# Optimization experiments

Hardware: AMD Instinct MI355X
Metric: run time of the kernel (lower is better)

The kernel has to match this reference:

```python
import jax, jax.numpy as jnp
import numpy as np

B, T, V, H, E, MAX_OOV = 128, 200, 50257, 256, 128, 50


def setup_inputs() -> dict:
    key = jax.random.key(0)
    ks = jax.random.split(key, 17)
    s = 0.05  # param scale
    return {
        "decoder_input": jax.random.randint(ks[0], (B, 1), 0, V),
        "encoder_outputs": jax.random.normal(ks[1], (B, T, 2 * H), jnp.float32),
        "encoder_idxs": jax.random.randint(ks[2], (B, T), 0, V),
        "prev_state": jax.random.normal(ks[3], (1, B, H), jnp.float32),
        "selective_read": jax.random.normal(ks[4], (B, 1, 2 * H), jnp.float32) * s,
        "step": 1,
        "emb": jax.random.normal(ks[5], (V, E), jnp.float32) * s,
        "W_ih": jax.random.normal(ks[6], (3 * H, E + 2 * H), jnp.float32) * s,
        "W_hh": jax.random.normal(ks[7], (3 * H, H), jnp.float32) * s,
        "b_ih": jax.random.normal(ks[8], (3 * H,), jnp.float32) * s,
        "b_hh": jax.random.normal(ks[9], (3 * H,), jnp.float32) * s,
        "Wi_w": jax.random.normal(ks[10], (H, 2 * H), jnp.float32) * s,
        "Wi_b": jax.random.normal(ks[11], (H,), jnp.float32) * s,
        "Wg_w": jax.random.normal(ks[12], (V, H), jnp.float32) * s,
        "Wg_b": jax.random.normal(ks[13], (V,), jnp.float32) * s,
        "Wc_w": jax.random.normal(ks[14], (H, 2 * H), jnp.float32) * s,
        "Wc_b": jax.random.normal(ks[15], (H,), jnp.float32) * s,
    }


def _gru_cell(x, h, W_ih, W_hh, b_ih, b_hh):
    # torch GRUCell math, gate order r,z,n
    gi = x @ W_ih.T + b_ih
    gh = h @ W_hh.T + b_hh
    i_r, i_z, i_n = jnp.split(gi, 3, axis=-1)
    h_r, h_z, h_n = jnp.split(gh, 3, axis=-1)
    r = jax.nn.sigmoid(i_r + h_r)
    z = jax.nn.sigmoid(i_z + h_z)
    n = jnp.tanh(i_n + r * h_n)
    return (1.0 - z) * n + z * h


def reference(decoder_input, encoder_outputs, encoder_idxs, prev_state, selective_read,
              step, emb, W_ih, W_hh, b_ih, b_hh, Wi_w, Wi_b, Wg_w, Wg_b, Wc_w, Wc_b):
    dtype = encoder_outputs.dtype
    if step == 0:
        prev_state = (encoder_outputs[:, -1] @ Wi_w.T + Wi_b)[None]      # 1,B,H
        selective_read = jnp.zeros((B, 1, 2 * H), dtype)
    embedded = emb[decoder_input[:, 0]]                                   # B,E
    gru_in = jnp.concatenate([selective_read[:, 0], embedded], axis=-1)   # B,2H+E
    decode_hidden = _gru_cell(gru_in, prev_state[0], W_ih, W_hh, b_ih, b_hh)  # B,H

    score_g = decode_hidden @ Wg_w.T + Wg_b                               # B,V
    enc_proj = jnp.tanh(jnp.einsum('bte,he->bth', encoder_outputs, Wc_w) + Wc_b)  # B,T,H
    score_c = jnp.tanh(jnp.einsum('bth,bh->bt', enc_proj, decode_hidden))         # B,T
    score_c = score_c + jnp.where(encoder_idxs == 0, -10000.0, 0.0).astype(dtype)

    probs = jax.nn.softmax(jnp.concatenate([score_g, score_c], axis=1), axis=1)   # B,V+T
    prob_g, prob_c = probs[:, :V], probs[:, V:]
    prob_g = jnp.concatenate([prob_g, jnp.full((B, MAX_OOV), 1e-4, dtype)], axis=1)  # B,V+oov

    # copy-distribution aggregation: scatter-add prob_c by vocab id (replaces one-hot bmm)
    prob_c_to_g = jnp.zeros((B, V + MAX_OOV), dtype).at[
        jnp.arange(B)[:, None], encoder_idxs].add(prob_c)
    prob_out = (prob_c_to_g + prob_g)[:, None, :]                          # B,1,V+oov

    # selective read for next step
    match = (encoder_idxs == decoder_input).astype(dtype)                  # B,T
    tot = match.sum(axis=1, keepdims=True)
    match = jnp.where(tot > 1, match / tot, match)
    prob_appeared = prob_c * match
    selective_read_new = jnp.einsum('bt,bte->be', prob_appeared, encoder_outputs)[:, None, :]  # B,1,2H
    return prob_out, decode_hidden, selective_read_new
```

## Files before the change

kernel.cpp:

```cpp
#include <hip/hip_runtime.h>

typedef __bf16 bf16;
typedef __bf16 bf16x8 __attribute__((ext_vector_type(8)));
typedef float f32x4 __attribute__((ext_vector_type(4)));

#define B_ 128
#define T_ 200
#define V_ 50257
#define H_ 256
#define E_ 128
#define OOV_ 50
#define VO_ 50307
#define NRG 80
#define NTS 5
#define GSC 629
#define TILES_G 3145
#define PSTR 3152
#define GPJ 400

__device__ __forceinline__ float sigmoid_(float x) { return 1.0f / (1.0f + __expf(-x)); }
__device__ __forceinline__ float tanh_(float x) { return 1.0f - 2.0f / (__expf(2.0f * x) + 1.0f); }

__global__ void k_front(const float* Wc_w, bf16* WcPack,
                        const int* step_p, const float* enc, const float* prev,
                        const float* selread, const int* dec, const float* emb,
                        const float* Wi_w, const float* Wi_b,
                        float* hT, float* ginT) {
    if (blockIdx.x < 128) {
        int gid = blockIdx.x * 256 + threadIdx.x;
        int n = gid >> 7;
        int k = (gid & 127) * 4;
        float4 v = *(const float4*)(Wc_w + n * 512 + k);
        int kstep = k >> 5, kin = k & 31;
        int q = kin >> 3, j0 = kin & 7;
        int r = n & 15, nt = n >> 4;
        int lane = q * 16 + r;
        bf16* d = WcPack + (((nt * 16 + kstep) * 64) + lane) * 8 + j0;
        d[0] = (bf16)v.x; d[1] = (bf16)v.y; d[2] = (bf16)v.z; d[3] = (bf16)v.w;
    } else {
        int b = blockIdx.x - 128, t = threadIdx.x;
        int step = step_p[0];
        float h;
        if (step == 0) {
            float acc = Wi_b[t];
            const float* er = enc + (b * T_ + (T_ - 1)) * 512;
            const float* wr = Wi_w + t * 512;
            for (int k = 0; k < 512; ++k) acc += er[k] * wr[k];
            h = acc;
        } else {
            h = prev[b * H_ + t];
        }
        hT[t * B_ + b] = h;
        for (int k = t; k < 512; k += 256)
            ginT[k * B_ + b] = (step == 0) ? 0.0f : selread[b * 512 + k];
        if (t < E_)
            ginT[(512 + t) * B_ + b] = emb[dec[b] * E_ + t];
    }
}

__global__ void k_gemm_gru(const float* W_ih, const float* b_ih,
                           const float* W_hh, const float* b_hh,
                           const float* ginT, const float* hT,
                           float* giT, float* ghT) {
    int g = blockIdx.x * 256 + threadIdx.x;
    int r = g >> 7, b = g & 127;
    const float* w = W_ih + r * 640;
    float a0 = 0.f, a1 = 0.f, a2 = 0.f, a3 = 0.f;
#pragma unroll 4
    for (int k = 0; k < 640; k += 4) {
        a0 += w[k]     * ginT[k * B_ + b];
        a1 += w[k + 1] * ginT[(k + 1) * B_ + b];
        a2 += w[k + 2] * ginT[(k + 2) * B_ + b];
        a3 += w[k + 3] * ginT[(k + 3) * B_ + b];
    }
    giT[r * B_ + b] = b_ih[r] + ((a0 + a1) + (a2 + a3));
    const float* w2 = W_hh + r * 256;
    float c0 = 0.f, c1 = 0.f, c2 = 0.f, c3 = 0.f;
#pragma unroll 4
    for (int k = 0; k < 256; k += 4) {
        c0 += w2[k]     * hT[k * B_ + b];
        c1 += w2[k + 1] * hT[(k + 1) * B_ + b];
        c2 += w2[k + 2] * hT[(k + 2) * B_ + b];
        c3 += w2[k + 3] * hT[(k + 3) * B_ + b];
    }
    ghT[r * B_ + b] = b_hh[r] + ((c0 + c1) + (c2 + c3));
}

__global__ void k_gru_cell(const float* giT, const float* ghT, const float* hT,
                           float* out_dh, bf16* Apack) {
    int b = blockIdx.x, j = threadIdx.x;
    float ir = giT[j * B_ + b], iz = giT[(256 + j) * B_ + b], in_ = giT[(512 + j) * B_ + b];
    float hr = ghT[j * B_ + b], hz = ghT[(256 + j) * B_ + b], hn = ghT[(512 + j) * B_ + b];
    float hp = hT[j * B_ + b];
    float r = sigmoid_(ir + hr);
    float z = sigmoid_(iz + hz);
    float n = tanh_(in_ + r * hn);
    float h = (1.0f - z) * n + z * hp;
    out_dh[b * H_ + j] = h;
    int mt = b >> 4, rr = b & 15, ks = j >> 5, q = (j >> 3) & 3, jj = j & 7;
    Apack[(((mt * 8 + ks) * 64) + (q * 16 + rr)) * 8 + jj] = (bf16)h;
}

__global__ __launch_bounds__(256, 3) void k_mm(const bf16* Apack, const float* Wg_w,
                                               const float* Wg_b, const float* enc,
                                               const bf16* WcPack, const float* Wc_b,
                                               const float* dh, const int* idxs,
                                               float* out_prob, float* pg_part, float* expc) {
    __shared__ unsigned char smem[43008];
    int tid = threadIdx.x;
    int w = tid >> 6, lane = tid & 63;
    int r = lane & 15, q = lane >> 4;
    if (blockIdx.x < GSC) {
        int blk = blockIdx.x;
        int n0 = blk * NRG;
        bf16* Bs = (bf16*)smem;
#pragma unroll
        for (int ph = 0; ph < 2; ++ph) {
            float4 tmp[10];
#pragma unroll
            for (int j = 0; j < 10; ++j) {
                int f = (ph * 10 + j) * 256 + tid;
                int row = f >> 6, c4 = f & 63;
                int n = n0 + row;
                tmp[j] = (n < V_) ? *(const float4*)(Wg_w + n * 256 + c4 * 4)
                                  : float4{0.f, 0.f, 0.f, 0.f};
            }
#pragma unroll
            for (int j = 0; j < 10; ++j) {
                int f = (ph * 10 + j) * 256 + tid;
                int row = f >> 6, c4 = f & 63;
                bf16* d = Bs + row * 264 + c4 * 4;
                d[0] = (bf16)tmp[j].x; d[1] = (bf16)tmp[j].y;
                d[2] = (bf16)tmp[j].z; d[3] = (bf16)tmp[j].w;
            }
        }
        bf16x8 a[2][8];
#pragma unroll
        for (int p = 0; p < 2; ++p)
#pragma unroll
            for (int ks = 0; ks < 8; ++ks)
                a[p][ks] = *(const bf16x8*)(Apack + ((2 * w + p) * 8 + ks) * 512 + lane * 8);
        __syncthreads();
        f32x4 acc[10];
#pragma unroll
        for (int i = 0; i < 10; ++i) acc[i] = (f32x4){0.f, 0.f, 0.f, 0.f};
#pragma unroll
        for (int ks = 0; ks < 8; ++ks) {
#pragma unroll
            for (int nt = 0; nt < NTS; ++nt) {
                bf16x8 bfr = *(const bf16x8*)(Bs + (nt * 16 + r) * 264 + ks * 32 + q * 8);
                acc[nt * 2]     = __builtin_amdgcn_mfma_f32_16x16x32_bf16(a[0][ks], bfr, acc[nt * 2], 0, 0, 0);
                acc[nt * 2 + 1] = __builtin_amdgcn_mfma_f32_16x16x32_bf16(a[1][ks], bfr, acc[nt * 2 + 1], 0, 0, 0);
            }
        }
        __syncthreads();
        float* Tr = (float*)smem;
#pragma unroll
        for (int nt = 0; nt < NTS; ++nt) {
            int n = n0 + nt * 16 + r;
            bool valid = n < V_;
            float wgb = valid ? Wg_b[n] : 0.0f;
#pragma unroll
            for (int p = 0; p < 2; ++p) {
#pragma unroll
                for (int rg = 0; rg < 4; ++rg) {
                    int row = (2 * w + p) * 16 + q * 4 + rg;
                    float e = valid ? __expf(acc[nt * 2 + p][rg] + wgb) : 0.0f;
                    Tr[row * 84 + nt * 16 + r] = e;
                    float sred = e;
                    sred += __shfl_xor(sred, 1);
                    sred += __shfl_xor(sred, 2);
                    sred += __shfl_xor(sred, 4);
                    sred += __shfl_xor(sred, 8);
                    if (r == 0) pg_part[row * PSTR + blk * NTS + nt] = sred;
                }
            }
        }
        __syncthreads();
        if (blk < GSC - 1) {
#pragma unroll
            for (int rnd = 0; rnd < 10; ++rnd) {
                int f = rnd * 256 + tid;
                int row = (f * 3277) >> 16;
                int c4 = f - row * 20;
                float4 v = *(const float4*)(Tr + row * 84 + c4 * 4);
                *(float4*)(out_prob + row * VO_ + n0 + c4 * 4) = v;
            }
        } else {
#pragma unroll
            for (int rnd = 0; rnd < 10; ++rnd) {
                int f = rnd * 256 + tid;
                int row = (f * 3277) >> 16;
                int c4 = f - row * 20;
#pragma unroll
                for (int i = 0; i < 4; ++i) {
                    int n = n0 + c4 * 4 + i;
                    if (n < V_) out_prob[row * VO_ + n] = Tr[row * 84 + c4 * 4 + i];
                }
            }
        }
    } else {
        int pblk = blockIdx.x - GSC;
        int m0 = pblk * 64;
        bf16* As = (bf16*)smem;
        float* sred = (float*)(smem + 33792);
        f32x4 acc[16];
#pragma unroll
        for (int i = 0; i < 16; ++i) acc[i] = (f32x4){0.f, 0.f, 0.f, 0.f};
        for (int half = 0; half < 2; ++half) {
            __syncthreads();
#pragma unroll
            for (int ph = 0; ph < 2; ++ph) {
                float4 tmp[8];
#pragma unroll
                for (int j = 0; j < 8; ++j) {
                    int f = (ph * 8 + j) * 256 + tid;
                    int row = f >> 6, c4 = f & 63;
                    tmp[j] = *(const float4*)(enc + (m0 + row) * 512 + half * 256 + c4 * 4);
                }
#pragma unroll
                for (int j = 0; j < 8; ++j) {
                    int f = (ph * 8 + j) * 256 + tid;
                    int row = f >> 6, c4 = f & 63;
                    bf16* d = As + row * 264 + c4 * 4;
                    d[0] = (bf16)tmp[j].x; d[1] = (bf16)tmp[j].y;
                    d[2] = (bf16)tmp[j].z; d[3] = (bf16)tmp[j].w;
                }
            }
            __syncthreads();
#pragma unroll
            for (int ks = 0; ks < 8; ++ks) {
                int kstep = half * 8 + ks;
                bf16x8 bfr[4];
#pragma unroll
                for (int ntl = 0; ntl < 4; ++ntl)
                    bfr[ntl] = *(const bf16x8*)(WcPack + (((w * 4 + ntl) * 16 + kstep) * 64 + lane) * 8);
#pragma unroll
                for (int mt = 0; mt < 4; ++mt) {
                    bf16x8 a = *(const bf16x8*)(As + (mt * 16 + r) * 264 + ks * 32 + q * 8);
#pragma unroll
                    for (int ntl = 0; ntl < 4; ++ntl)
                        acc[mt * 4 + ntl] = __builtin_amdgcn_mfma_f32_16x16x32_bf16(a, bfr[ntl], acc[mt * 4 + ntl], 0, 0, 0);
                }
            }
        }
#pragma unroll
        for (int mt = 0; mt < 4; ++mt) {
#pragma unroll
            for (int rg = 0; rg < 4; ++rg) {
                int rowl = mt * 16 + q * 4 + rg;
                int row = m0 + rowl;
                int b = row / T_;
                float s = 0.0f;
#pragma unroll
                for (int ntl = 0; ntl < 4; ++ntl) {
                    int n = (w * 4 + ntl) * 16 + r;
                    float pv = tanh_(acc[mt * 4 + ntl][rg] + Wc_b[n]);
                    s += pv * dh[b * H_ + n];
                }
                s += __shfl_xor(s, 1);
                s += __shfl_xor(s, 2);
                s += __shfl_xor(s, 4);
                s += __shfl_xor(s, 8);
                if (r == 0) sred[rowl * 4 + w] = s;
            }
        }
        __syncthreads();
        if (tid < 64) {
            float s = sred[tid * 4] + sred[tid * 4 + 1] + sred[tid * 4 + 2] + sred[tid * 4 + 3];
            int row = m0 + tid;
            int b = row / T_, t = row - b * T_;
            float sc = tanh_(s);
            if (idxs[b * T_ + t] == 0) sc -= 10000.0f;
            expc[row] = __expf(sc);
        }
    }
}

__global__ void k_red_scatter(const float* pg_part, const float* expc_, const int* idxs,
                              const int* dec, const float* enc, float* inv_out,
                              float* out_prob, float* out_sel) {
    __shared__ float red[256];
    __shared__ float cf[256];
    int b = blockIdx.x, t = threadIdx.x;
    float s = 0.0f;
    for (int i = t; i < TILES_G; i += 256) s += pg_part[b * PSTR + i];
    if (t < T_) s += expc_[b * T_ + t];
    red[t] = s;
    __syncthreads();
    for (int k = 128; k > 0; k >>= 1) {
        if (t < k) red[t] += red[t + k];
        __syncthreads();
    }
    float iv = 1.0f / red[0];
    if (t == 0) inv_out[b] = iv;
    __syncthreads();
    int d = dec[b];
    float ec = 0.0f;
    int m = 0;
    if (t < T_) {
        int ix = idxs[b * T_ + t];
        ec = expc_[b * T_ + t];
        atomicAdd(&out_prob[b * VO_ + ix], ec);
        m = (ix == d) ? 1 : 0;
    }
    cf[t] = m ? ec * iv : 0.0f;
    red[t] = m ? 1.0f : 0.0f;
    __syncthreads();
    for (int k = 128; k > 0; k >>= 1) {
        if (t < k) red[t] += red[t + k];
        __syncthreads();
    }
    float tot = red[0];
    float scale = (tot > 1.0f) ? 1.0f / tot : 1.0f;
    float a0 = 0.0f, a1 = 0.0f;
    for (int tt = 0; tt < T_; ++tt) {
        float c = cf[tt];
        if (c != 0.0f) {
            float wgt = c * scale;
            a0 += wgt * enc[(b * T_ + tt) * 512 + t];
            a1 += wgt * enc[(b * T_ + tt) * 512 + t + 256];
        }
    }
    out_sel[b * 512 + t] = a0;
    out_sel[b * 512 + t + 256] = a1;
}

__global__ void k_norm(float* out_prob, const float* inv) {
    int i4 = blockIdx.x * 256 + threadIdx.x;
    if (i4 >= (B_ * VO_ / 4)) return;
    float4 vv = ((const float4*)out_prob)[i4];
    float r[4];
    int base = i4 * 4;
#pragma unroll
    for (int c = 0; c < 4; ++c) {
        int idx = base + c;
        int b = idx / VO_;
        int v = idx - b * VO_;
        float x = (c == 0) ? vv.x : (c == 1) ? vv.y : (c == 2) ? vv.z : vv.w;
        r[c] = (v < V_) ? x * inv[b] : 1e-4f;
    }
    ((float4*)out_prob)[i4] = make_float4(r[0], r[1], r[2], r[3]);
}

extern "C" void kernel_launch(void* const* d_in, const int* in_sizes, int n_in,
                              void* d_out, int out_size, void* d_ws, size_t ws_size,
                              hipStream_t stream) {
    const int*   dec     = (const int*)d_in[0];
    const float* enc     = (const float*)d_in[1];
    const int*   idxs    = (const int*)d_in[2];
    const float* prev    = (const float*)d_in[3];
    const float* selread = (const float*)d_in[4];
    const int*   step_p  = (const int*)d_in[5];
    const float* emb     = (const float*)d_in[6];
    const float* W_ih    = (const float*)d_in[7];
    const float* W_hh    = (const float*)d_in[8];
    const float* b_ih    = (const float*)d_in[9];
    const float* b_hh    = (const float*)d_in[10];
    const float* Wi_w    = (const float*)d_in[11];
    const float* Wi_b    = (const float*)d_in[12];
    const float* Wg_w    = (const float*)d_in[13];
    const float* Wg_b    = (const float*)d_in[14];
    const float* Wc_w    = (const float*)d_in[15];
    const float* Wc_b    = (const float*)d_in[16];

    float* ws     = (float*)d_ws;
    float* hT     = ws;
    float* ginT   = ws + 32768;
    float* giT    = ws + 114688;
    float* ghT    = ws + 212992;
    float* inv    = ws + 311296;
    float* expc   = ws + 311552;
    float* pgp    = ws + 337152;
    bf16*  Apack  = (bf16*)(ws + 741376);
    bf16*  WcPack = (bf16*)(ws + 757760);

    float* out      = (float*)d_out;
    float* out_prob = out;
    float* out_dh   = out + 6439296;
    float* out_sel  = out + 6439296 + 32768;

    k_front<<<256, 256, 0, stream>>>(Wc_w, WcPack, step_p, enc, prev, selread, dec,
                                     emb, Wi_w, Wi_b, hT, ginT);
    k_gemm_gru<<<384, 256, 0, stream>>>(W_ih, b_ih, W_hh, b_hh, ginT, hT, giT, ghT);
    k_gru_cell<<<B_, 256, 0, stream>>>(giT, ghT, hT, out_dh, Apack);
    k_mm<<<GSC + GPJ, 256, 0, stream>>>(Apack, Wg_w, Wg_b, enc, WcPack, Wc_b,
                                        out_dh, idxs, out_prob, pgp, expc);
    k_red_scatter<<<B_, 256, 0, stream>>>(pgp, expc, idxs, dec, enc, inv, out_prob, out_sel);
    k_norm<<<(B_ * VO_ / 4 + 255) / 256, 256, 0, stream>>>(out_prob, inv);
}
```

Before: 271.3 us.

## Make k_mm persistent with double-buffered LDS tiles and register prefetch

Turns the generator-score and copy-projection halves of k_mm into persistent loops over smaller 32-row chunks. Each iteration prefetches the next chunk's fp32 weights or encoder rows into registers while the MFMAs run on the current LDS buffer, then writes them to the other buffer. The launch shrinks to a fixed 1024 blocks and LDS use drops, so the occupancy hint rises from 3 to 4 blocks per CU. The staged LDS transpose before the output store is removed in favour of direct scalar stores of the exponentials, which gives up the coalesced float4 writes.

```diff
diff --git a/kernel.cpp b/kernel.cpp
--- a/kernel.cpp
+++ b/kernel.cpp
@@ -11,12 +11,12 @@
 #define E_ 128
 #define OOV_ 50
 #define VO_ 50307
-#define NRG 80
-#define NTS 5
-#define GSC 629
-#define TILES_G 3145
+#define NCH_S 1571
+#define NCH_P 800
+#define SB 512
+#define PB 512
+#define TILES_G 3142
 #define PSTR 3152
-#define GPJ 400
 
 __device__ __forceinline__ float sigmoid_(float x) { return 1.0f / (1.0f + __expf(-x)); }
 __device__ __forceinline__ float tanh_(float x) { return 1.0f - 2.0f / (__expf(2.0f * x) + 1.0f); }
@@ -101,178 +101,206 @@
     Apack[(((mt * 8 + ks) * 64) + (q * 16 + rr)) * 8 + jj] = (bf16)h;
 }
 
-__global__ __launch_bounds__(256, 3) void k_mm(const bf16* Apack, const float* Wg_w,
+__global__ __launch_bounds__(256, 4) void k_mm(const bf16* Apack, const float* Wg_w,
                                                const float* Wg_b, const float* enc,
                                                const bf16* WcPack, const float* Wc_b,
                                                const float* dh, const int* idxs,
                                                float* out_prob, float* pg_part, float* expc) {
-    __shared__ unsigned char smem[43008];
+    __shared__ unsigned char smem[34816];
+    bf16* buf0 = (bf16*)smem;
+    bf16* buf1 = (bf16*)(smem + 16896);
+    float* sredp = (float*)(smem + 33792);
     int tid = threadIdx.x;
     int w = tid >> 6, lane = tid & 63;
     int r = lane & 15, q = lane >> 4;
-    if (blockIdx.x < GSC) {
+    if (blockIdx.x < SB) {
         int blk = blockIdx.x;
-        int n0 = blk * NRG;
-        bf16* Bs = (bf16*)smem;
-#pragma unroll
-        for (int ph = 0; ph < 2; ++ph) {
-            float4 tmp[10];
-#pragma unroll
-            for (int j = 0; j < 10; ++j) {
-                int f = (ph * 10 + j) * 256 + tid;
+        bf16x8 a[2][8];
+#pragma unroll
+        for (int p = 0; p < 2; ++p)
+#pragma unroll
+            for (int ks = 0; ks < 8; ++ks)
+                a[p][ks] = *(const bf16x8*)(Apack + ((2 * w + p) * 8 + ks) * 512 + lane * 8);
+        {
+            int n0 = blk * 32;
+#pragma unroll
+            for (int j = 0; j < 8; ++j) {
+                int f = j * 256 + tid;
                 int row = f >> 6, c4 = f & 63;
                 int n = n0 + row;
-                tmp[j] = (n < V_) ? *(const float4*)(Wg_w + n * 256 + c4 * 4)
-                                  : float4{0.f, 0.f, 0.f, 0.f};
-            }
-#pragma unroll
-            for (int j = 0; j < 10; ++j) {
-                int f = (ph * 10 + j) * 256 + tid;
-                int row = f >> 6, c4 = f & 63;
-                bf16* d = Bs + row * 264 + c4 * 4;
-                d[0] = (bf16)tmp[j].x; d[1] = (bf16)tmp[j].y;
-                d[2] = (bf16)tmp[j].z; d[3] = (bf16)tmp[j].w;
-            }
-        }
-        bf16x8 a[2][8];
-#pragma unroll
-        for (int p = 0; p < 2; ++p)
-#pragma unroll
-            for (int ks = 0; ks < 8; ++ks)
-                a[p][ks] = *(const bf16x8*)(Apack + ((2 * w + p) * 8 + ks) * 512 + lane * 8);
-        __syncthreads();
-        f32x4 acc[10];
-#pragma unroll
-        for (int i = 0; i < 10; ++i) acc[i] = (f32x4){0.f, 0.f, 0.f, 0.f};
-#pragma unroll
-        for (int ks = 0; ks < 8; ++ks) {
-#pragma unroll
-            for (int nt = 0; nt < NTS; ++nt) {
-                bf16x8 bfr = *(const bf16x8*)(Bs + (nt * 16 + r) * 264 + ks * 32 + q * 8);
-                acc[nt * 2]     = __builtin_amdgcn_mfma_f32_16x16x32_bf16(a[0][ks], bfr, acc[nt * 2], 0, 0, 0);
-                acc[nt * 2 + 1] = __builtin_amdgcn_mfma_f32_16x16x32_bf16(a[1][ks], bfr, acc[nt * 2 + 1], 0, 0, 0);
-            }
-        }
-        __syncthreads();
-        float* Tr = (float*)smem;
-#pragma unroll
-        for (int nt = 0; nt < NTS; ++nt) {
-            int n = n0 + nt * 16 + r;
-            bool valid = n < V_;
-            float wgb = valid ? Wg_b[n] : 0.0f;
-#pragma unroll
-            for (int p = 0; p < 2; ++p) {
-#pragma unroll
-                for (int rg = 0; rg < 4; ++rg) {
-                    int row = (2 * w + p) * 16 + q * 4 + rg;
-                    float e = valid ? __expf(acc[nt * 2 + p][rg] + wgb) : 0.0f;
-                    Tr[row * 84 + nt * 16 + r] = e;
-                    float sred = e;
-                    sred += __shfl_xor(sred, 1);
-                    sred += __shfl_xor(sred, 2);
-                    sred += __shfl_xor(sred, 4);
-                    sred += __shfl_xor(sred, 8);
-                    if (r == 0) pg_part[row * PSTR + blk * NTS + nt] = sred;
-                }
-            }
-        }
-        __syncthreads();
-        if (blk < GSC - 1) {
-#pragma unroll
-            for (int rnd = 0; rnd < 10; ++rnd) {
-                int f = rnd * 256 + tid;
-                int row = (f * 3277) >> 16;
-                int c4 = f - row * 20;
-                float4 v = *(const float4*)(Tr + row * 84 + c4 * 4);
-                *(float4*)(out_prob + row * VO_ + n0 + c4 * 4) = v;
-            }
-        } else {
-#pragma unroll
-            for (int rnd = 0; rnd < 10; ++rnd) {
-                int f = rnd * 256 + tid;
-                int row = (f * 3277) >> 16;
-                int c4 = f - row * 20;
-#pragma unroll
-                for (int i = 0; i < 4; ++i) {
-                    int n = n0 + c4 * 4 + i;
-                    if (n < V_) out_prob[row * VO_ + n] = Tr[row * 84 + c4 * 4 + i];
-                }
-            }
-        }
-    } else {
-        int pblk = blockIdx.x - GSC;
-        int m0 = pblk * 64;
-        bf16* As = (bf16*)smem;
-        float* sred = (float*)(smem + 33792);
-        f32x4 acc[16];
-#pragma unroll
-        for (int i = 0; i < 16; ++i) acc[i] = (f32x4){0.f, 0.f, 0.f, 0.f};
-        for (int half = 0; half < 2; ++half) {
+                float4 v = (n < V_) ? *(const float4*)(Wg_w + n * 256 + c4 * 4)
+                                    : float4{0.f, 0.f, 0.f, 0.f};
+                bf16* d = buf0 + row * 264 + c4 * 4;
+                d[0] = (bf16)v.x; d[1] = (bf16)v.y; d[2] = (bf16)v.z; d[3] = (bf16)v.w;
+            }
+        }
+        int cur = 0;
+        for (int c = blk; c < NCH_S; c += SB) {
+            int n0 = c * 32;
+            int cn = c + SB;
+            bool hn = cn < NCH_S;
+            float4 tmp[8];
+            if (hn) {
+                int n0n = cn * 32;
+#pragma unroll
+                for (int j = 0; j < 8; ++j) {
+                    int f = j * 256 + tid;
+                    int row = f >> 6, c4 = f & 63;
+                    int n = n0n + row;
+                    tmp[j] = (n < V_) ? *(const float4*)(Wg_w + n * 256 + c4 * 4)
+                                      : float4{0.f, 0.f, 0.f, 0.f};
+                }
+            }
             __syncthreads();
-#pragma unroll
-            for (int ph = 0; ph < 2; ++ph) {
-                float4 tmp[8];
+            const bf16* Bq = cur ? buf1 : buf0;
+            f32x4 acc[4];
+#pragma unroll
+            for (int i = 0; i < 4; ++i) acc[i] = (f32x4){0.f, 0.f, 0.f, 0.f};
+#pragma unroll
+            for (int ks = 0; ks < 8; ++ks) {
+#pragma unroll
+                for (int ntl = 0; ntl < 2; ++ntl) {
+                    bf16x8 bfr = *(const bf16x8*)(Bq + (ntl * 16 + r) * 264 + ks * 32 + q * 8);
+                    acc[ntl * 2]     = __builtin_amdgcn_mfma_f32_16x16x32_bf16(a[0][ks], bfr, acc[ntl * 2], 0, 0, 0);
+                    acc[ntl * 2 + 1] = __builtin_amdgcn_mfma_f32_16x16x32_bf16(a[1][ks], bfr, acc[ntl * 2 + 1], 0, 0, 0);
+                }
+            }
+            if (hn) {
+                bf16* Bn = cur ? buf0 : buf1;
 #pragma unroll
                 for (int j = 0; j < 8; ++j) {
-                    int f = (ph * 8 + j) * 256 + tid;
+                    int f = j * 256 + tid;
                     int row = f >> 6, c4 = f & 63;
-                    tmp[j] = *(const float4*)(enc + (m0 + row) * 512 + half * 256 + c4 * 4);
-                }
-#pragma unroll
-                for (int j = 0; j < 8; ++j) {
-                    int f = (ph * 8 + j) * 256 + tid;
-                    int row = f >> 6, c4 = f & 63;
-                    bf16* d = As + row * 264 + c4 * 4;
+                    bf16* d = Bn + row * 264 + c4 * 4;
                     d[0] = (bf16)tmp[j].x; d[1] = (bf16)tmp[j].y;
                     d[2] = (bf16)tmp[j].z; d[3] = (bf16)tmp[j].w;
                 }
             }
+#pragma unroll
+            for (int ntl = 0; ntl < 2; ++ntl) {
+                int n = n0 + ntl * 16 + r;
+                bool valid = n < V_;
+                float wgb = valid ? Wg_b[n] : 0.0f;
+#pragma unroll
+                for (int p = 0; p < 2; ++p) {
+#pragma unroll
+                    for (int rg = 0; rg < 4; ++rg) {
+                        int row = (2 * w + p) * 16 + q * 4 + rg;
+                        float e = valid ? __expf(acc[ntl * 2 + p][rg] + wgb) : 0.0f;
+                        if (valid) out_prob[row * VO_ + n] = e;
+                        float sr = e;
+                        sr += __shfl_xor(sr, 1);
+                        sr += __shfl_xor(sr, 2);
+                        sr += __shfl_xor(sr, 4);
+                        sr += __shfl_xor(sr, 8);
+                        if (r == 0) pg_part[row * PSTR + c * 2 + ntl] = sr;
+                    }
+                }
+            }
+            cur ^= 1;
+        }
+    } else {
+        int pblk = blockIdx.x - SB;
+        int nc = 0;
+        for (int c = pblk; c < NCH_P; c += PB) ++nc;
+        int nhc = nc * 2;
+        {
+            int m0 = pblk * 32;
+#pragma unroll
+            for (int j = 0; j < 8; ++j) {
+                int f = j * 256 + tid;
+                int row = f >> 6, c4 = f & 63;
+                float4 v = *(const float4*)(enc + (m0 + row) * 512 + c4 * 4);
+                bf16* d = buf0 + row * 264 + c4 * 4;
+                d[0] = (bf16)v.x; d[1] = (bf16)v.y; d[2] = (bf16)v.z; d[3] = (bf16)v.w;
+            }
+        }
+        int cur = 0;
+        f32x4 acc[8];
+        for (int i = 0; i < nhc; ++i) {
+            int ch = pblk + (i >> 1) * PB;
+            int h = i & 1;
+            int m0 = ch * 32;
+            bool hn = i + 1 < nhc;
+            float4 tmp[8];
+            if (hn) {
+                int chn = pblk + ((i + 1) >> 1) * PB;
+                int h2 = (i + 1) & 1;
+                int m0n = chn * 32;
+#pragma unroll
+                for (int j = 0; j < 8; ++j) {
+                    int f = j * 256 + tid;
+                    int row = f >> 6, c4 = f & 63;
+                    tmp[j] = *(const float4*)(enc + (m0n + row) * 512 + h2 * 256 + c4 * 4);
+                }
+            }
             __syncthreads();
+            const bf16* Bq = cur ? buf1 : buf0;
+            if (h == 0) {
+#pragma unroll
+                for (int k = 0; k < 8; ++k) acc[k] = (f32x4){0.f, 0.f, 0.f, 0.f};
+            }
 #pragma unroll
             for (int ks = 0; ks < 8; ++ks) {
-                int kstep = half * 8 + ks;
+                int ksg = h * 8 + ks;
                 bf16x8 bfr[4];
 #pragma unroll
                 for (int ntl = 0; ntl < 4; ++ntl)
-                    bfr[ntl] = *(const bf16x8*)(WcPack + (((w * 4 + ntl) * 16 + kstep) * 64 + lane) * 8);
-#pragma unroll
-                for (int mt = 0; mt < 4; ++mt) {
-                    bf16x8 a = *(const bf16x8*)(As + (mt * 16 + r) * 264 + ks * 32 + q * 8);
+                    bfr[ntl] = *(const bf16x8*)(WcPack + (((w * 4 + ntl) * 16 + ksg) * 64 + lane) * 8);
+#pragma unroll
+                for (int mtl = 0; mtl < 2; ++mtl) {
+                    bf16x8 av = *(const bf16x8*)(Bq + (mtl * 16 + r) * 264 + ks * 32 + q * 8);
 #pragma unroll
                     for (int ntl = 0; ntl < 4; ++ntl)
-                        acc[mt * 4 + ntl] = __builtin_amdgcn_mfma_f32_16x16x32_bf16(a, bfr[ntl], acc[mt * 4 + ntl], 0, 0, 0);
-                }
-            }
-        }
-#pragma unroll
-        for (int mt = 0; mt < 4; ++mt) {
-#pragma unroll
-            for (int rg = 0; rg < 4; ++rg) {
-                int rowl = mt * 16 + q * 4 + rg;
-                int row = m0 + rowl;
-                int b = row / T_;
-                float s = 0.0f;
-#pragma unroll
-                for (int ntl = 0; ntl < 4; ++ntl) {
-                    int n = (w * 4 + ntl) * 16 + r;
-                    float pv = tanh_(acc[mt * 4 + ntl][rg] + Wc_b[n]);
-                    s += pv * dh[b * H_ + n];
-                }
-                s += __shfl_xor(s, 1);
-                s += __shfl_xor(s, 2);
-                s += __shfl_xor(s, 4);
-                s += __shfl_xor(s, 8);
-                if (r == 0) sred[rowl * 4 + w] = s;
-            }
-        }
-        __syncthreads();
-        if (tid < 64) {
-            float s = sred[tid * 4] + sred[tid * 4 + 1] + sred[tid * 4 + 2] + sred[tid * 4 + 3];
-            int row = m0 + tid;
-            int b = row / T_, t = row - b * T_;
-            float sc = tanh_(s);
-            if (idxs[b * T_ + t] == 0) sc -= 10000.0f;
-            expc[row] = __expf(sc);
+                        acc[mtl * 4 + ntl] = __builtin_amdgcn_mfma_f32_16x16x32_bf16(av, bfr[ntl], acc[mtl * 4 + ntl], 0, 0, 0);
+                }
+            }
+            if (hn) {
+                bf16* Bn = cur ? buf0 : buf1;
+#pragma unroll
+                for (int j = 0; j < 8; ++j) {
+                    int f = j * 256 + tid;
+                    int row = f >> 6, c4 = f & 63;
+                    bf16* d = Bn + row * 264 + c4 * 4;
+                    d[0] = (bf16)tmp[j].x; d[1] = (bf16)tmp[j].y;
+                    d[2] = (bf16)tmp[j].z; d[3] = (bf16)tmp[j].w;
+                }
+            }
+            if (h == 1) {
+                int par = (i >> 1) & 1;
+#pragma unroll
+                for (int mtl = 0; mtl < 2; ++mtl) {
+#pragma unroll
+                    for (int rg = 0; rg < 4; ++rg) {
+                        int rowl = mtl * 16 + q * 4 + rg;
+                        int row = m0 + rowl;
+                        int b = row / T_;
+                        float s = 0.0f;
+#pragma unroll
+                        for (int ntl = 0; ntl < 4; ++ntl) {
+                            int n = (w * 4 + ntl) * 16 + r;
+                            float pv = tanh_(acc[mtl * 4 + ntl][rg] + Wc_b[n]);
+                            s += pv * dh[b * H_ + n];
+                        }
+                        s += __shfl_xor(s, 1);
+                        s += __shfl_xor(s, 2);
+                        s += __shfl_xor(s, 4);
+                        s += __shfl_xor(s, 8);
+                        if (r == 0) sredp[par * 128 + rowl * 4 + w] = s;
+                    }
+                }
+                __syncthreads();
+                if (tid < 32) {
+                    float s = sredp[par * 128 + tid * 4]     + sredp[par * 128 + tid * 4 + 1]
+                            + sredp[par * 128 + tid * 4 + 2] + sredp[par * 128 + tid * 4 + 3];
+                    int row = m0 + tid;
+                    int b = row / T_, t = row - b * T_;
+                    float sc = tanh_(s);
+                    if (idxs[b * T_ + t] == 0) sc -= 10000.0f;
+                    expc[row] = __expf(sc);
+                }
+            }
+            cur ^= 1;
         }
     }
 }
@@ -384,8 +412,8 @@
                                      emb, Wi_w, Wi_b, hT, ginT);
     k_gemm_gru<<<384, 256, 0, stream>>>(W_ih, b_ih, W_hh, b_hh, ginT, hT, giT, ghT);
     k_gru_cell<<<B_, 256, 0, stream>>>(giT, ghT, hT, out_dh, Apack);
-    k_mm<<<GSC + GPJ, 256, 0, stream>>>(Apack, Wg_w, Wg_b, enc, WcPack, Wc_b,
-                                        out_dh, idxs, out_prob, pgp, expc);
+    k_mm<<<SB + PB, 256, 0, stream>>>(Apack, Wg_w, Wg_b, enc, WcPack, Wc_b,
+                                      out_dh, idxs, out_prob, pgp, expc);
     k_red_scatter<<<B_, 256, 0, stream>>>(pgp, expc, idxs, dec, enc, inv, out_prob, out_sel);
     k_norm<<<(B_ * VO_ / 4 + 255) / 256, 256, 0, stream>>>(out_prob, inv);
 }
```

Result: slower. 316.8 us (+16.8%).
